# Performance work log

Measured on AMD Instinct MI355X. Metric: run time of the kernel, lower is better.

Reference implementation:

```python
import jax, jax.numpy as jnp
import numpy as np

B = 8192          # sessions
DOCS = 10         # docs per session
NPS = 21          # nodes per session: 1 query + 10 docs + 10 titles
N = B * NPS       # 172032 total nodes
F_IN, F_HID, F_OUT = 171, 256, 128


def _gat_conv(x, src, dst, W, a_src, a_dst, bias, n_nodes):
    # PyG GATConv, heads=1, negative_slope=0.2, self-loops already appended.
    h = x @ W.T                                   # [N, F]
    e = jax.nn.leaky_relu(jnp.take(h @ a_src, src) + jnp.take(h @ a_dst, dst), 0.2)
    m = jax.ops.segment_max(e, dst, num_segments=n_nodes)
    ex = jnp.exp(e - m[dst])
    denom = jax.ops.segment_sum(ex, dst, num_segments=n_nodes)
    alpha = ex / denom[dst]                       # softmax over incoming edges
    out = jax.ops.segment_sum(h[src] * alpha[:, None], dst, num_segments=n_nodes)
    return out + bias


def setup_inputs() -> dict:
    key = jax.random.key(0)
    ks = jax.random.split(key, 20)
    # structured node ids: per session block [q, d0..d9, t0..t9]
    base = jnp.arange(B, dtype=jnp.int64) * NPS
    doc_id = base[:, None] + 1 + jnp.arange(DOCS, dtype=jnp.int64)   # [B,10]
    q = base                                                          # query node = doc_id[:,0]-1
    t = doc_id + DOCS                                                 # title node = doc+10
    qd_s = jnp.repeat(q, DOCS); qd_d = doc_id.reshape(-1)
    dt_s = doc_id.reshape(-1);  dt_d = t.reshape(-1)
    src = jnp.concatenate([qd_s, qd_d, dt_s, dt_d])
    dst = jnp.concatenate([qd_d, qd_s, dt_d, dt_s])
    edge_index = jnp.stack([src, dst])                                # [2, 327680]

    inp = {
        "i": 0,
        "x": jax.random.normal(ks[0], (N, F_IN), jnp.float32),
        "edge_index": edge_index,
        "doc_id": doc_id,
        "click": jax.random.randint(ks[1], (B,), 0, 2),
        "query": jax.random.randint(ks[2], (B,), 0, 6338),
        "docu": jax.random.randint(ks[3], (B, DOCS), 0, 56477),
        "title_id": jax.random.randint(ks[4], (B, DOCS), 0, 56363),
        # embedding tables
        "query_table": jax.random.normal(ks[5], (6338, 160), jnp.float32) * 0.02,
        "doc_table": jax.random.normal(ks[6], (56477, 160), jnp.float32) * 0.02,
        "title_table": jax.random.normal(ks[7], (56363, 160), jnp.float32) * 0.02,
        "pos_table": jax.random.normal(ks[8], (10, 1), jnp.float32) * 0.02,
        "click_table": jax.random.normal(ks[9], (2, 1), jnp.float32) * 0.02,
        # GATConv 1 (171 -> 256)
        "W1": jax.random.normal(ks[10], (F_HID, F_IN), jnp.float32) * (1.0 / np.sqrt(F_IN)),
        "a_src1": jax.random.normal(ks[11], (F_HID,), jnp.float32) * 0.1,
        "a_dst1": jax.random.normal(ks[12], (F_HID,), jnp.float32) * 0.1,
        "b1": jnp.zeros((F_HID,), jnp.float32),
        # GATConv 2 (256 -> 128)
        "W2": jax.random.normal(ks[13], (F_OUT, F_HID), jnp.float32) * (1.0 / np.sqrt(F_HID)),
        "a_src2": jax.random.normal(ks[14], (F_OUT,), jnp.float32) * 0.1,
        "a_dst2": jax.random.normal(ks[15], (F_OUT,), jnp.float32) * 0.1,
        "b2": jnp.zeros((F_OUT,), jnp.float32),
        # head linear (128 -> 1)
        "Wl": jax.random.normal(ks[16], (1, F_OUT), jnp.float32) * (1.0 / np.sqrt(F_OUT)),
        "bl": jnp.zeros((1,), jnp.float32),
    }
    return inp


def reference(i, x, edge_index, doc_id, click, query, docu, title_id,
              query_table, doc_table, title_table, pos_table, click_table,
              W1, a_src1, a_dst1, b1, W2, a_src2, a_dst2, b2, Wl, bl):
    n_nodes = x.shape[0]
    q_emb = query_table[query]          # [B,160]
    d_emb = doc_table[docu]             # [B,10,160]
    t_emb = title_table[title_id]       # [B,10,160]
    pos = pos_table[:, 0]               # [10]  (position_embedding of 0..9)
    clk = click_table[click, 0]         # [B]

    df = doc_id.reshape(-1)             # flat doc node ids [B*10]
    if i == 0:
        x = x.at[doc_id[:, 0] - 1, :160].set(q_emb)
        x = x.at[df, :160].set(d_emb.reshape(-1, 160))
        x = x.at[df, 160].set(jnp.broadcast_to(pos, doc_id.shape).reshape(-1))
        x = x.at[df, 161 + i].set(jnp.broadcast_to(clk[:, None], doc_id.shape).reshape(-1))
        x = x.at[df + 10, :160].set(t_emb.reshape(-1, 160))
    else:
        x = x.at[df, 161 + i].set(jnp.broadcast_to(clk[:, None], doc_id.shape).reshape(-1))

    # add self-loops (PyG GATConv default)
    loop = jnp.arange(n_nodes, dtype=edge_index.dtype)
    src = jnp.concatenate([edge_index[0], loop])
    dst = jnp.concatenate([edge_index[1], loop])

    y = _gat_conv(x, src, dst, W1, a_src1, a_dst1, b1, n_nodes)
    y = jax.nn.relu(y)                  # dropout is identity in eval mode
    hidden_state = _gat_conv(y, src, dst, W2, a_src2, a_dst2, b2, n_nodes)
    y = jax.nn.relu(hidden_state)
    y = jax.nn.sigmoid(y @ Wl.T + bl)   # [N,1]
    return (hidden_state, y, x[:, :171])
```

## Files before the change

### kernel.cpp

```cpp
#include <hip/hip_runtime.h>
#include <cstdint>

#define N_NODES 172032
#define BATCH   8192
#define NPS     21
#define F_IN    171
#define K1P     192
#define F_HID   256
#define F_OUT   128
#define SX_F    (NPS * F_IN)
#define SXB     (NPS * K1P)
#define SPB     3
#define NBLK    2731

typedef unsigned short u16;
typedef __attribute__((ext_vector_type(8))) short  bf16x8;
typedef __attribute__((ext_vector_type(4))) float  f32x4;

__device__ inline u16 f2bf(float f) {
    unsigned u = __float_as_uint(f);
    unsigned r = u + 0x7FFFu + ((u >> 16) & 1u);
    return (u16)(r >> 16);
}
__device__ inline float bf2f(u16 h) { return __uint_as_float(((unsigned)h) << 16); }
__device__ inline float lrelu(float v) { return v > 0.f ? v : 0.2f * v; }

__device__ inline int deg_of(int n)  { return n == 0 ? 11 : (n <= 10 ? 3 : 2); }
__device__ inline int edge_base(int n) { return n == 0 ? 0 : (n <= 10 ? 11 + 3*(n-1) : 41 + 2*(n-11)); }
__device__ inline int src_of(int n, int k) {
    if (n == 0)  return k < 10 ? k + 1 : 0;
    if (n <= 10) return k == 0 ? 0 : (k == 1 ? n + 10 : n);
    return k == 0 ? n - 10 : n;
}

__device__ inline float wave_red(float v) {
    for (int off = 32; off; off >>= 1) v += __shfl_down(v, off);
    return v;
}

__global__ __launch_bounds__(256) void build_x(const int* __restrict__ iptr, const float* __restrict__ x,
                        const int* __restrict__ click, const int* __restrict__ query,
                        const int* __restrict__ docu, const int* __restrict__ title_id,
                        const float* __restrict__ qtab, const float* __restrict__ dtab,
                        const float* __restrict__ ttab, const float* __restrict__ ptab,
                        const float* __restrict__ ctab,
                        const float* __restrict__ W1, const float* __restrict__ W2,
                        float* __restrict__ out_x, u16* __restrict__ xb,
                        u16* __restrict__ W1b, u16* __restrict__ W2b)
{
    if (blockIdx.x >= BATCH) {
        int id = (blockIdx.x - BATCH) * 256 + threadIdx.x;
        if (id < 256 * K1P) {
            int r = id / K1P, k = id - r * K1P;
            W1b[id] = (k < F_IN) ? f2bf(W1[r * F_IN + k]) : (u16)0;
        }
        if (id < 128 * 256) W2b[id] = f2bf(W2[id]);
        return;
    }

    __shared__ float sx[SX_F];
    __shared__ int   dz[10], tz[10], s_q;
    __shared__ float s_clk;

    const int s   = blockIdx.x;
    const int tid = threadIdx.x;
    const int i   = iptr[0];
    const long xbase = (long)s * SX_F;

    if (tid < 10)       dz[tid]      = docu[s*10 + tid];
    else if (tid < 20)  tz[tid - 10] = title_id[s*10 + tid - 10];
    else if (tid == 20) s_q          = query[s];
    else if (tid == 21) s_clk        = ctab[click[s]];
    __syncthreads();

    if (i == 0) {
        for (int idx = tid; idx < SX_F; idx += 256) {
            int p = idx / F_IN;
            int c = idx - p * F_IN;
            float v;
            if (c >= 160) {
                if (p >= 1 && p <= 10 && c == 160)      v = ptab[p - 1];
                else if (p >= 1 && p <= 10 && c == 161) v = s_clk;
                else                                     v = x[xbase + idx];
            } else {
                if (p == 0)       v = qtab[(long)s_q * 160 + c];
                else if (p <= 10) v = dtab[(long)dz[p-1] * 160 + c];
                else              v = ttab[(long)tz[p-11] * 160 + c];
            }
            sx[idx] = v;
        }
    } else {
        for (int idx = tid; idx < SX_F; idx += 256) {
            int p = idx / F_IN;
            int c = idx - p * F_IN;
            float v = x[xbase + idx];
            if (p >= 1 && p <= 10 && c == 161 + i) v = s_clk;
            sx[idx] = v;
        }
    }
    __syncthreads();

    {
        int r    = (int)(xbase & 3);
        int head = (4 - r) & 3;
        if (tid < head) out_x[xbase + tid] = sx[tid];
        int n4 = (SX_F - head) >> 2;
        for (int id = tid; id < n4; id += 256) {
            int o = head + id * 4;
            float4 v = make_float4(sx[o], sx[o+1], sx[o+2], sx[o+3]);
            *(float4*)(out_x + xbase + o) = v;
        }
        int done = head + n4 * 4;
        int tail = SX_F - done;
        if (tid < tail) out_x[xbase + done + tid] = sx[done + tid];
    }

    {
        u16* xbs = xb + (long)s * SXB;
        for (int id = tid; id < SXB / 8; id += 256) {
            int k0 = id * 8;
            int node = k0 / K1P;
            int kk   = k0 - node * K1P;
            union { u16 h[8]; uint4 v; } u;
            #pragma unroll
            for (int j = 0; j < 8; ++j) {
                int c = kk + j;
                u.h[j] = (c < F_IN) ? f2bf(sx[node * F_IN + c]) : (u16)0;
            }
            *(uint4*)(xbs + k0) = u.v;
        }
    }
}

__global__ __launch_bounds__(256) void fused1(const u16* __restrict__ xb, const u16* __restrict__ W1b,
                                              const float* __restrict__ asrc, const float* __restrict__ adst,
                                              const float* __restrict__ bias, u16* __restrict__ y1b)
{
    constexpr int KS  = 64;
    constexpr int SA  = 200;
    constexpr int SB  = 72;
    __shared__ __align__(16) u16 Al[64 * SA];
    __shared__ __align__(16) u16 Bu[256 * SB];
    __shared__ float s_l[64], d_l[64], alpha[3 * 61];

    const int blk = blockIdx.x, tid = threadIdx.x;
    const int s0  = blk * SPB;
    const int nsamp = (s0 + SPB <= BATCH) ? SPB : (BATCH - s0);
    const int nrow  = nsamp * NPS;

    const int lane = tid & 63, w = tid >> 6;
    const int wr = w >> 1, wc = w & 1;
    const int lm = lane & 15, lq = lane >> 4;

    const u16* Ag = xb + (long)s0 * SXB;
    for (int id = tid; id < 64 * (K1P / 8); id += 256) {
        int row = id / 24, ch = id - row * 24;
        uint4 v;
        if (row < nrow) v = *(const uint4*)(Ag + row * K1P + ch * 8);
        else            v = make_uint4(0u, 0u, 0u, 0u);
        *(uint4*)(Al + row * SA + ch * 8) = v;
    }

    f32x4 acc[2][8];
    #pragma unroll
    for (int f = 0; f < 2; ++f)
        #pragma unroll
        for (int g = 0; g < 8; ++g)
            acc[f][g] = (f32x4){0.f, 0.f, 0.f, 0.f};

    for (int ks = 0; ks < K1P; ks += KS) {
        __syncthreads();
        for (int id = tid; id < 256 * (KS / 8); id += 256) {
            int row = id >> 3, ch = id & 7;
            *(uint4*)(Bu + row * SB + ch * 8) = *(const uint4*)(W1b + row * K1P + ks + ch * 8);
        }
        __syncthreads();
        #pragma unroll
        for (int kb = 0; kb < KS / 32; ++kb) {
            int ka    = ks + kb * 32 + lq * 8;
            int kboff = kb * 32 + lq * 8;
            bf16x8 a0 = *(const bf16x8*)(Al + (wr*32 +  0 + lm) * SA + ka);
            bf16x8 a1 = *(const bf16x8*)(Al + (wr*32 + 16 + lm) * SA + ka);
            #pragma unroll
            for (int g = 0; g < 8; ++g) {
                bf16x8 b = *(const bf16x8*)(Bu + (wc*128 + g*16 + lm) * SB + kboff);
                acc[0][g] = __builtin_amdgcn_mfma_f32_16x16x32_bf16(a0, b, acc[0][g], 0, 0, 0);
                acc[1][g] = __builtin_amdgcn_mfma_f32_16x16x32_bf16(a1, b, acc[1][g], 0, 0, 0);
            }
        }
    }

    __syncthreads();
    u16* h = Bu;
    #pragma unroll
    for (int f = 0; f < 2; ++f)
        #pragma unroll
        for (int g = 0; g < 8; ++g)
            #pragma unroll
            for (int r = 0; r < 4; ++r) {
                int row = wr*32 + f*16 + lq*4 + r;
                int col = wc*128 + g*16 + lm;
                h[row * F_HID + col] = f2bf(acc[f][g][r]);
            }
    __syncthreads();

    float av[4], dv[4];
    #pragma unroll
    for (int j = 0; j < 4; ++j) { av[j] = asrc[lane + j*64]; dv[j] = adst[lane + j*64]; }
    for (int n = w; n < nrow; n += 4) {
        float as_ = 0.f, ad_ = 0.f;
        #pragma unroll
        for (int j = 0; j < 4; ++j) {
            float hv = bf2f(h[n * F_HID + lane + j*64]);
            as_ += hv * av[j];
            ad_ += hv * dv[j];
        }
        as_ = wave_red(as_); ad_ = wave_red(ad_);
        if (lane == 0) { s_l[n] = as_; d_l[n] = ad_; }
    }
    __syncthreads();

    if (tid < nrow) {
        int s = tid / NPS, p = tid - s * NPS;
        int deg = deg_of(p), eb = edge_base(p);
        const float* sl = s_l + s * NPS;
        float dn = d_l[tid], m = -1e30f;
        for (int k = 0; k < deg; ++k) m = fmaxf(m, lrelu(sl[src_of(p,k)] + dn));
        float den = 0.f;
        for (int k = 0; k < deg; ++k) den += expf(lrelu(sl[src_of(p,k)] + dn) - m);
        float inv = 1.f / den;
        for (int k = 0; k < deg; ++k) alpha[s*61 + eb + k] = expf(lrelu(sl[src_of(p,k)] + dn) - m) * inv;
    }
    __syncthreads();

    const int c = tid;
    float bc = bias[c];
    for (int s = 0; s < nsamp; ++s) {
        const u16* hs = h + s * NPS * F_HID;
        const float* al = alpha + s * 61;
        u16* outp = y1b + ((long)(s0 + s) * NPS) * F_HID;
        {
            float a = al[10] * bf2f(hs[c]);
            #pragma unroll
            for (int j = 1; j <= 10; ++j) a += al[j-1] * bf2f(hs[j * F_HID + c]);
            outp[c] = f2bf(fmaxf(a + bc, 0.f));
        }
        #pragma unroll
        for (int j = 1; j <= 10; ++j) {
            int eb = 11 + 3*(j-1);
            float a = al[eb]   * bf2f(hs[c])
                    + al[eb+1] * bf2f(hs[(j+10) * F_HID + c])
                    + al[eb+2] * bf2f(hs[j * F_HID + c]);
            outp[j * F_HID + c] = f2bf(fmaxf(a + bc, 0.f));
        }
        #pragma unroll
        for (int j = 1; j <= 10; ++j) {
            int eb = 41 + 2*(j-1);
            float a = al[eb]   * bf2f(hs[j * F_HID + c])
                    + al[eb+1] * bf2f(hs[(10+j) * F_HID + c]);
            outp[(10+j) * F_HID + c] = f2bf(fmaxf(a + bc, 0.f));
        }
    }
}

__global__ __launch_bounds__(256) void fused2(const u16* __restrict__ y1b, const u16* __restrict__ W2b,
                                              const float* __restrict__ asrc, const float* __restrict__ adst,
                                              const float* __restrict__ bias,
                                              const float* __restrict__ Wl, const float* __restrict__ bl,
                                              float* __restrict__ out_hid, float* __restrict__ out_y)
{
    constexpr int KS  = 64;
    constexpr int SA  = 264;
    constexpr int SB  = 72;
    __shared__ __align__(16) u16 Al[64 * SA];
    __shared__ __align__(16) u16 Bu[128 * SB];
    __shared__ float s_l[64], d_l[64], alpha[3 * 61];

    const int blk = blockIdx.x, tid = threadIdx.x;
    const int s0  = blk * SPB;
    const int nsamp = (s0 + SPB <= BATCH) ? SPB : (BATCH - s0);
    const int nrow  = nsamp * NPS;

    const int lane = tid & 63, w = tid >> 6;
    const int wr = w >> 1, wc = w & 1;
    const int lm = lane & 15, lq = lane >> 4;

    const u16* Ag = y1b + (long)s0 * NPS * F_HID;
    for (int id = tid; id < 64 * (F_HID / 8); id += 256) {
        int row = id >> 5, ch = id & 31;
        uint4 v;
        if (row < nrow) v = *(const uint4*)(Ag + row * F_HID + ch * 8);
        else            v = make_uint4(0u, 0u, 0u, 0u);
        *(uint4*)(Al + row * SA + ch * 8) = v;
    }

    f32x4 acc[2][4];
    #pragma unroll
    for (int f = 0; f < 2; ++f)
        #pragma unroll
        for (int g = 0; g < 4; ++g)
            acc[f][g] = (f32x4){0.f, 0.f, 0.f, 0.f};

    for (int ks = 0; ks < F_HID; ks += KS) {
        __syncthreads();
        for (int id = tid; id < 128 * (KS / 8); id += 256) {
            int row = id >> 3, ch = id & 7;
            *(uint4*)(Bu + row * SB + ch * 8) = *(const uint4*)(W2b + row * F_HID + ks + ch * 8);
        }
        __syncthreads();
        #pragma unroll
        for (int kb = 0; kb < KS / 32; ++kb) {
            int ka    = ks + kb * 32 + lq * 8;
            int kboff = kb * 32 + lq * 8;
            bf16x8 a0 = *(const bf16x8*)(Al + (wr*32 +  0 + lm) * SA + ka);
            bf16x8 a1 = *(const bf16x8*)(Al + (wr*32 + 16 + lm) * SA + ka);
            #pragma unroll
            for (int g = 0; g < 4; ++g) {
                bf16x8 b = *(const bf16x8*)(Bu + (wc*64 + g*16 + lm) * SB + kboff);
                acc[0][g] = __builtin_amdgcn_mfma_f32_16x16x32_bf16(a0, b, acc[0][g], 0, 0, 0);
                acc[1][g] = __builtin_amdgcn_mfma_f32_16x16x32_bf16(a1, b, acc[1][g], 0, 0, 0);
            }
        }
    }

    __syncthreads();
    u16* h2 = Bu;
    #pragma unroll
    for (int f = 0; f < 2; ++f)
        #pragma unroll
        for (int g = 0; g < 4; ++g)
            #pragma unroll
            for (int r = 0; r < 4; ++r) {
                int row = wr*32 + f*16 + lq*4 + r;
                int col = wc*64 + g*16 + lm;
                h2[row * F_OUT + col] = f2bf(acc[f][g][r]);
            }
    __syncthreads();

    float av[2], dv[2];
    #pragma unroll
    for (int j = 0; j < 2; ++j) { av[j] = asrc[lane + j*64]; dv[j] = adst[lane + j*64]; }
    for (int n = w; n < nrow; n += 4) {
        float as_ = 0.f, ad_ = 0.f;
        #pragma unroll
        for (int j = 0; j < 2; ++j) {
            float hv = bf2f(h2[n * F_OUT + lane + j*64]);
            as_ += hv * av[j];
            ad_ += hv * dv[j];
        }
        as_ = wave_red(as_); ad_ = wave_red(ad_);
        if (lane == 0) { s_l[n] = as_; d_l[n] = ad_; }
    }
    __syncthreads();

    if (tid < nrow) {
        int s = tid / NPS, p = tid - s * NPS;
        int deg = deg_of(p), eb = edge_base(p);
        const float* sl = s_l + s * NPS;
        float dn = d_l[tid], m = -1e30f;
        for (int k = 0; k < deg; ++k) m = fmaxf(m, lrelu(sl[src_of(p,k)] + dn));
        float den = 0.f;
        for (int k = 0; k < deg; ++k) den += expf(lrelu(sl[src_of(p,k)] + dn) - m);
        float inv = 1.f / den;
        for (int k = 0; k < deg; ++k) alpha[s*61 + eb + k] = expf(lrelu(sl[src_of(p,k)] + dn) - m) * inv;
    }
    __syncthreads();

    float* hidwl = (float*)Al;
    const int c    = tid & 127;
    const int half = tid >> 7;
    float bc = bias[c];
    float wl = Wl[c];
    for (int s = 0; s < nsamp; ++s) {
        const u16* hs = h2 + s * NPS * F_OUT;
        const float* al = alpha + s * 61;
        long gb = (long)(s0 + s) * NPS * F_OUT;
        for (int p = half; p < NPS; p += 2) {
            int deg = deg_of(p), eb = edge_base(p);
            float a = 0.f;
            for (int k = 0; k < deg; ++k) a += al[eb + k] * bf2f(hs[src_of(p,k) * F_OUT + c]);
            float hv = a + bc;
            out_hid[gb + p * F_OUT + c] = hv;
            hidwl[(s * NPS + p) * F_OUT + c] = fmaxf(hv, 0.f) * wl;
        }
    }
    __syncthreads();

    float bl0 = bl[0];
    for (int n = w; n < nrow; n += 4) {
        float v = hidwl[n * F_OUT + lane] + hidwl[n * F_OUT + lane + 64];
        v = wave_red(v);
        if (lane == 0) out_y[(long)s0 * NPS + n] = 1.f / (1.f + expf(-(v + bl0)));
    }
}

extern "C" void kernel_launch(void* const* d_in, const int* in_sizes, int n_in,
                              void* d_out, int out_size, void* d_ws, size_t ws_size,
                              hipStream_t stream) {
    const int*   ip    = (const int*)  d_in[0];
    const float* x     = (const float*)d_in[1];
    const int*   click = (const int*)  d_in[4];
    const int*   query = (const int*)  d_in[5];
    const int*   docu  = (const int*)  d_in[6];
    const int*   title = (const int*)  d_in[7];
    const float* qtab  = (const float*)d_in[8];
    const float* dtab  = (const float*)d_in[9];
    const float* ttab  = (const float*)d_in[10];
    const float* ptab  = (const float*)d_in[11];
    const float* ctab  = (const float*)d_in[12];
    const float* W1    = (const float*)d_in[13];
    const float* as1   = (const float*)d_in[14];
    const float* ad1   = (const float*)d_in[15];
    const float* b1    = (const float*)d_in[16];
    const float* W2    = (const float*)d_in[17];
    const float* as2   = (const float*)d_in[18];
    const float* ad2   = (const float*)d_in[19];
    const float* b2    = (const float*)d_in[20];
    const float* Wl    = (const float*)d_in[21];
    const float* bl    = (const float*)d_in[22];

    float* out_hid = (float*)d_out;
    float* out_y   = out_hid + (long)N_NODES * F_OUT;
    float* out_x   = out_y + N_NODES;

    u16* xb  = (u16*)d_ws;
    u16* y1b = xb + (long)BATCH * SXB;
    u16* W1b = y1b + (long)N_NODES * F_HID;
    u16* W2b = W1b + 256 * K1P;

    build_x<<<BATCH + 192, 256, 0, stream>>>(ip, x, click, query, docu, title,
                                             qtab, dtab, ttab, ptab, ctab,
                                             W1, W2, out_x, xb, W1b, W2b);
    fused1<<<NBLK, 256, 0, stream>>>(xb, W1b, as1, ad1, b1, y1b);
    fused2<<<NBLK, 256, 0, stream>>>(y1b, W2b, as2, ad2, b2, Wl, bl, out_hid, out_y);
}
```

Measured before the change: 645.5 us.

## Read GEMM weights from global memory, fuse attention logits into epilogue, pad LDS

Both fused GAT kernels stop staging weight tiles through shared memory with a sync-heavy k loop. They now read W1b/W2b fragments directly from global memory or L2, and shared memory holds only the activation tile, so occupancy can rise (launch bounds now request 4 blocks). The attention source and destination dot products are computed from MFMA accumulators with shuffle reductions instead of a separate pass over LDS, and the softmax caches exponentials. The prep kernel pads the shared row stride and gathers embeddings with float4 loads, and the final linear head reduces per wave without an extra LDS buffer. In exchange, each wave repeatedly fetches weights from global memory, which relies on cache hits.

```diff
diff --git a/kernel.cpp b/kernel.cpp
--- a/kernel.cpp
+++ b/kernel.cpp
@@ -9,6 +9,7 @@
 #define F_HID   256
 #define F_OUT   128
 #define SX_F    (NPS * F_IN)
+#define SXP     172
 #define SXB     (NPS * K1P)
 #define SPB     3
 #define NBLK    2731
@@ -58,7 +59,7 @@
         return;
     }
 
-    __shared__ float sx[SX_F];
+    __shared__ float sx[NPS * SXP];
     __shared__ int   dz[10], tz[10], s_q;
     __shared__ float s_clk;
 
@@ -74,20 +75,21 @@
     __syncthreads();
 
     if (i == 0) {
-        for (int idx = tid; idx < SX_F; idx += 256) {
-            int p = idx / F_IN;
-            int c = idx - p * F_IN;
+        for (int id = tid; id < NPS * 40; id += 256) {
+            int p = id / 40, c4 = (id - p * 40) * 4;
+            const float* src;
+            if (p == 0)       src = qtab + (long)s_q * 160;
+            else if (p <= 10) src = dtab + (long)dz[p-1] * 160;
+            else              src = ttab + (long)tz[p-11] * 160;
+            *(float4*)(sx + p * SXP + c4) = *(const float4*)(src + c4);
+        }
+        for (int id = tid; id < NPS * 11; id += 256) {
+            int p = id / 11, c = 160 + (id - p * 11);
             float v;
-            if (c >= 160) {
-                if (p >= 1 && p <= 10 && c == 160)      v = ptab[p - 1];
-                else if (p >= 1 && p <= 10 && c == 161) v = s_clk;
-                else                                     v = x[xbase + idx];
-            } else {
-                if (p == 0)       v = qtab[(long)s_q * 160 + c];
-                else if (p <= 10) v = dtab[(long)dz[p-1] * 160 + c];
-                else              v = ttab[(long)tz[p-11] * 160 + c];
-            }
-            sx[idx] = v;
+            if (p >= 1 && p <= 10 && c == 160)      v = ptab[p - 1];
+            else if (p >= 1 && p <= 10 && c == 161) v = s_clk;
+            else                                     v = x[xbase + p * F_IN + c];
+            sx[p * SXP + c] = v;
         }
     } else {
         for (int idx = tid; idx < SX_F; idx += 256) {
@@ -95,7 +97,7 @@
             int c = idx - p * F_IN;
             float v = x[xbase + idx];
             if (p >= 1 && p <= 10 && c == 161 + i) v = s_clk;
-            sx[idx] = v;
+            sx[p * SXP + c] = v;
         }
     }
     __syncthreads();
@@ -103,16 +105,33 @@
     {
         int r    = (int)(xbase & 3);
         int head = (4 - r) & 3;
-        if (tid < head) out_x[xbase + tid] = sx[tid];
+        if (tid < head) {
+            int p = tid / F_IN, c = tid - p * F_IN;
+            out_x[xbase + tid] = sx[p * SXP + c];
+        }
         int n4 = (SX_F - head) >> 2;
         for (int id = tid; id < n4; id += 256) {
             int o = head + id * 4;
-            float4 v = make_float4(sx[o], sx[o+1], sx[o+2], sx[o+3]);
+            float4 v;
+            {
+                int p0 = o / F_IN, c0 = o - p0 * F_IN;
+                v.x = sx[p0 * SXP + c0];
+                int o1 = o + 1; int p1 = o1 / F_IN, c1 = o1 - p1 * F_IN;
+                v.y = sx[p1 * SXP + c1];
+                int o2 = o + 2; int p2 = o2 / F_IN, c2 = o2 - p2 * F_IN;
+                v.z = sx[p2 * SXP + c2];
+                int o3 = o + 3; int p3 = o3 / F_IN, c3 = o3 - p3 * F_IN;
+                v.w = sx[p3 * SXP + c3];
+            }
             *(float4*)(out_x + xbase + o) = v;
         }
         int done = head + n4 * 4;
         int tail = SX_F - done;
-        if (tid < tail) out_x[xbase + done + tid] = sx[done + tid];
+        if (tid < tail) {
+            int idx = done + tid;
+            int p = idx / F_IN, c = idx - p * F_IN;
+            out_x[xbase + idx] = sx[p * SXP + c];
+        }
     }
 
     {
@@ -125,23 +144,21 @@
             #pragma unroll
             for (int j = 0; j < 8; ++j) {
                 int c = kk + j;
-                u.h[j] = (c < F_IN) ? f2bf(sx[node * F_IN + c]) : (u16)0;
+                u.h[j] = (c < F_IN) ? f2bf(sx[node * SXP + c]) : (u16)0;
             }
             *(uint4*)(xbs + k0) = u.v;
         }
     }
 }
 
-__global__ __launch_bounds__(256) void fused1(const u16* __restrict__ xb, const u16* __restrict__ W1b,
-                                              const float* __restrict__ asrc, const float* __restrict__ adst,
-                                              const float* __restrict__ bias, u16* __restrict__ y1b)
+__global__ __launch_bounds__(256, 4) void fused1(const u16* __restrict__ xb, const u16* __restrict__ W1b,
+                                                 const float* __restrict__ asrc, const float* __restrict__ adst,
+                                                 const float* __restrict__ bias, u16* __restrict__ y1b)
 {
-    constexpr int KS  = 64;
-    constexpr int SA  = 200;
-    constexpr int SB  = 72;
-    __shared__ __align__(16) u16 Al[64 * SA];
-    __shared__ __align__(16) u16 Bu[256 * SB];
-    __shared__ float s_l[64], d_l[64], alpha[3 * 61];
+    constexpr int SA = 200;
+    __shared__ __align__(16) u16 hbuf[64 * 256];
+    __shared__ float s_part[2][64], d_part[2][64];
+    __shared__ float alpha[SPB * 61];
 
     const int blk = blockIdx.x, tid = threadIdx.x;
     const int s0  = blk * SPB;
@@ -153,13 +170,14 @@
     const int lm = lane & 15, lq = lane >> 4;
 
     const u16* Ag = xb + (long)s0 * SXB;
-    for (int id = tid; id < 64 * (K1P / 8); id += 256) {
+    for (int id = tid; id < 64 * 24; id += 256) {
         int row = id / 24, ch = id - row * 24;
         uint4 v;
         if (row < nrow) v = *(const uint4*)(Ag + row * K1P + ch * 8);
         else            v = make_uint4(0u, 0u, 0u, 0u);
-        *(uint4*)(Al + row * SA + ch * 8) = v;
-    }
+        *(uint4*)(hbuf + row * SA + ch * 8) = v;
+    }
+    __syncthreads();
 
     f32x4 acc[2][8];
     #pragma unroll
@@ -168,68 +186,65 @@
         for (int g = 0; g < 8; ++g)
             acc[f][g] = (f32x4){0.f, 0.f, 0.f, 0.f};
 
-    for (int ks = 0; ks < K1P; ks += KS) {
-        __syncthreads();
-        for (int id = tid; id < 256 * (KS / 8); id += 256) {
-            int row = id >> 3, ch = id & 7;
-            *(uint4*)(Bu + row * SB + ch * 8) = *(const uint4*)(W1b + row * K1P + ks + ch * 8);
-        }
-        __syncthreads();
-        #pragma unroll
-        for (int kb = 0; kb < KS / 32; ++kb) {
-            int ka    = ks + kb * 32 + lq * 8;
-            int kboff = kb * 32 + lq * 8;
-            bf16x8 a0 = *(const bf16x8*)(Al + (wr*32 +  0 + lm) * SA + ka);
-            bf16x8 a1 = *(const bf16x8*)(Al + (wr*32 + 16 + lm) * SA + ka);
+    #pragma unroll
+    for (int kb = 0; kb < K1P / 32; ++kb) {
+        int koff = kb * 32 + lq * 8;
+        bf16x8 a0 = *(const bf16x8*)(hbuf + (wr*32 +  0 + lm) * SA + koff);
+        bf16x8 a1 = *(const bf16x8*)(hbuf + (wr*32 + 16 + lm) * SA + koff);
+        #pragma unroll
+        for (int g = 0; g < 8; ++g) {
+            bf16x8 b = *(const bf16x8*)(W1b + (wc*128 + g*16 + lm) * K1P + koff);
+            acc[0][g] = __builtin_amdgcn_mfma_f32_16x16x32_bf16(a0, b, acc[0][g], 0, 0, 0);
+            acc[1][g] = __builtin_amdgcn_mfma_f32_16x16x32_bf16(a1, b, acc[1][g], 0, 0, 0);
+        }
+    }
+    __syncthreads();
+
+    u16* h = hbuf;
+    float av[8], dv[8];
+    #pragma unroll
+    for (int g = 0; g < 8; ++g) {
+        av[g] = asrc[wc*128 + g*16 + lm];
+        dv[g] = adst[wc*128 + g*16 + lm];
+    }
+    #pragma unroll
+    for (int f = 0; f < 2; ++f)
+        #pragma unroll
+        for (int r = 0; r < 4; ++r) {
+            int row = wr*32 + f*16 + lq*4 + r;
+            float sp = 0.f, dp = 0.f;
             #pragma unroll
             for (int g = 0; g < 8; ++g) {
-                bf16x8 b = *(const bf16x8*)(Bu + (wc*128 + g*16 + lm) * SB + kboff);
-                acc[0][g] = __builtin_amdgcn_mfma_f32_16x16x32_bf16(a0, b, acc[0][g], 0, 0, 0);
-                acc[1][g] = __builtin_amdgcn_mfma_f32_16x16x32_bf16(a1, b, acc[1][g], 0, 0, 0);
-            }
-        }
-    }
-
-    __syncthreads();
-    u16* h = Bu;
-    #pragma unroll
-    for (int f = 0; f < 2; ++f)
-        #pragma unroll
-        for (int g = 0; g < 8; ++g)
-            #pragma unroll
-            for (int r = 0; r < 4; ++r) {
-                int row = wr*32 + f*16 + lq*4 + r;
-                int col = wc*128 + g*16 + lm;
-                h[row * F_HID + col] = f2bf(acc[f][g][r]);
-            }
-    __syncthreads();
-
-    float av[4], dv[4];
-    #pragma unroll
-    for (int j = 0; j < 4; ++j) { av[j] = asrc[lane + j*64]; dv[j] = adst[lane + j*64]; }
-    for (int n = w; n < nrow; n += 4) {
-        float as_ = 0.f, ad_ = 0.f;
-        #pragma unroll
-        for (int j = 0; j < 4; ++j) {
-            float hv = bf2f(h[n * F_HID + lane + j*64]);
-            as_ += hv * av[j];
-            ad_ += hv * dv[j];
-        }
-        as_ = wave_red(as_); ad_ = wave_red(ad_);
-        if (lane == 0) { s_l[n] = as_; d_l[n] = ad_; }
-    }
+                float v = acc[f][g][r];
+                h[row * F_HID + wc*128 + g*16 + lm] = f2bf(v);
+                sp += v * av[g];
+                dp += v * dv[g];
+            }
+            #pragma unroll
+            for (int off = 1; off < 16; off <<= 1) {
+                sp += __shfl_xor(sp, off);
+                dp += __shfl_xor(dp, off);
+            }
+            if (lm == 0) { s_part[wc][row] = sp; d_part[wc][row] = dp; }
+        }
     __syncthreads();
 
     if (tid < nrow) {
         int s = tid / NPS, p = tid - s * NPS;
         int deg = deg_of(p), eb = edge_base(p);
-        const float* sl = s_l + s * NPS;
-        float dn = d_l[tid], m = -1e30f;
-        for (int k = 0; k < deg; ++k) m = fmaxf(m, lrelu(sl[src_of(p,k)] + dn));
+        int sb = s * NPS;
+        float dn = d_part[0][tid] + d_part[1][tid];
+        float e[11];
+        float m = -1e30f;
+        for (int k = 0; k < deg; ++k) {
+            int sn = sb + src_of(p, k);
+            e[k] = lrelu(s_part[0][sn] + s_part[1][sn] + dn);
+            m = fmaxf(m, e[k]);
+        }
         float den = 0.f;
-        for (int k = 0; k < deg; ++k) den += expf(lrelu(sl[src_of(p,k)] + dn) - m);
+        for (int k = 0; k < deg; ++k) { e[k] = expf(e[k] - m); den += e[k]; }
         float inv = 1.f / den;
-        for (int k = 0; k < deg; ++k) alpha[s*61 + eb + k] = expf(lrelu(sl[src_of(p,k)] + dn) - m) * inv;
+        for (int k = 0; k < deg; ++k) alpha[s*61 + eb + k] = e[k] * inv;
     }
     __syncthreads();
 
@@ -263,18 +278,17 @@
     }
 }
 
-__global__ __launch_bounds__(256) void fused2(const u16* __restrict__ y1b, const u16* __restrict__ W2b,
-                                              const float* __restrict__ asrc, const float* __restrict__ adst,
-                                              const float* __restrict__ bias,
-                                              const float* __restrict__ Wl, const float* __restrict__ bl,
-                                              float* __restrict__ out_hid, float* __restrict__ out_y)
+__global__ __launch_bounds__(256, 4) void fused2(const u16* __restrict__ y1b, const u16* __restrict__ W2b,
+                                                 const float* __restrict__ asrc, const float* __restrict__ adst,
+                                                 const float* __restrict__ bias,
+                                                 const float* __restrict__ Wl, const float* __restrict__ bl,
+                                                 float* __restrict__ out_hid, float* __restrict__ out_y)
 {
-    constexpr int KS  = 64;
-    constexpr int SA  = 264;
-    constexpr int SB  = 72;
-    __shared__ __align__(16) u16 Al[64 * SA];
-    __shared__ __align__(16) u16 Bu[128 * SB];
-    __shared__ float s_l[64], d_l[64], alpha[3 * 61];
+    constexpr int SA = 264;
+    __shared__ __align__(16) u16 hbuf[64 * SA];
+    __shared__ float s_part[2][64], d_part[2][64];
+    __shared__ float alpha[SPB * 61];
+    __shared__ float rpart[SPB * NPS][2];
 
     const int blk = blockIdx.x, tid = threadIdx.x;
     const int s0  = blk * SPB;
@@ -286,13 +300,14 @@
     const int lm = lane & 15, lq = lane >> 4;
 
     const u16* Ag = y1b + (long)s0 * NPS * F_HID;
-    for (int id = tid; id < 64 * (F_HID / 8); id += 256) {
+    for (int id = tid; id < 64 * 32; id += 256) {
         int row = id >> 5, ch = id & 31;
         uint4 v;
         if (row < nrow) v = *(const uint4*)(Ag + row * F_HID + ch * 8);
         else            v = make_uint4(0u, 0u, 0u, 0u);
-        *(uint4*)(Al + row * SA + ch * 8) = v;
-    }
+        *(uint4*)(hbuf + row * SA + ch * 8) = v;
+    }
+    __syncthreads();
 
     f32x4 acc[2][4];
     #pragma unroll
@@ -301,72 +316,68 @@
         for (int g = 0; g < 4; ++g)
             acc[f][g] = (f32x4){0.f, 0.f, 0.f, 0.f};
 
-    for (int ks = 0; ks < F_HID; ks += KS) {
-        __syncthreads();
-        for (int id = tid; id < 128 * (KS / 8); id += 256) {
-            int row = id >> 3, ch = id & 7;
-            *(uint4*)(Bu + row * SB + ch * 8) = *(const uint4*)(W2b + row * F_HID + ks + ch * 8);
-        }
-        __syncthreads();
-        #pragma unroll
-        for (int kb = 0; kb < KS / 32; ++kb) {
-            int ka    = ks + kb * 32 + lq * 8;
-            int kboff = kb * 32 + lq * 8;
-            bf16x8 a0 = *(const bf16x8*)(Al + (wr*32 +  0 + lm) * SA + ka);
-            bf16x8 a1 = *(const bf16x8*)(Al + (wr*32 + 16 + lm) * SA + ka);
+    #pragma unroll
+    for (int kb = 0; kb < F_HID / 32; ++kb) {
+        int koff = kb * 32 + lq * 8;
+        bf16x8 a0 = *(const bf16x8*)(hbuf + (wr*32 +  0 + lm) * SA + koff);
+        bf16x8 a1 = *(const bf16x8*)(hbuf + (wr*32 + 16 + lm) * SA + koff);
+        #pragma unroll
+        for (int g = 0; g < 4; ++g) {
+            bf16x8 b = *(const bf16x8*)(W2b + (wc*64 + g*16 + lm) * F_HID + koff);
+            acc[0][g] = __builtin_amdgcn_mfma_f32_16x16x32_bf16(a0, b, acc[0][g], 0, 0, 0);
+            acc[1][g] = __builtin_amdgcn_mfma_f32_16x16x32_bf16(a1, b, acc[1][g], 0, 0, 0);
+        }
+    }
+    __syncthreads();
+
+    u16* h2 = hbuf;
+    float av[4], dv[4];
+    #pragma unroll
+    for (int g = 0; g < 4; ++g) {
+        av[g] = asrc[wc*64 + g*16 + lm];
+        dv[g] = adst[wc*64 + g*16 + lm];
+    }
+    #pragma unroll
+    for (int f = 0; f < 2; ++f)
+        #pragma unroll
+        for (int r = 0; r < 4; ++r) {
+            int row = wr*32 + f*16 + lq*4 + r;
+            float sp = 0.f, dp = 0.f;
             #pragma unroll
             for (int g = 0; g < 4; ++g) {
-                bf16x8 b = *(const bf16x8*)(Bu + (wc*64 + g*16 + lm) * SB + kboff);
-                acc[0][g] = __builtin_amdgcn_mfma_f32_16x16x32_bf16(a0, b, acc[0][g], 0, 0, 0);
-                acc[1][g] = __builtin_amdgcn_mfma_f32_16x16x32_bf16(a1, b, acc[1][g], 0, 0, 0);
-            }
-        }
-    }
-
-    __syncthreads();
-    u16* h2 = Bu;
-    #pragma unroll
-    for (int f = 0; f < 2; ++f)
-        #pragma unroll
-        for (int g = 0; g < 4; ++g)
-            #pragma unroll
-            for (int r = 0; r < 4; ++r) {
-                int row = wr*32 + f*16 + lq*4 + r;
-                int col = wc*64 + g*16 + lm;
-                h2[row * F_OUT + col] = f2bf(acc[f][g][r]);
-            }
-    __syncthreads();
-
-    float av[2], dv[2];
-    #pragma unroll
-    for (int j = 0; j < 2; ++j) { av[j] = asrc[lane + j*64]; dv[j] = adst[lane + j*64]; }
-    for (int n = w; n < nrow; n += 4) {
-        float as_ = 0.f, ad_ = 0.f;
-        #pragma unroll
-        for (int j = 0; j < 2; ++j) {
-            float hv = bf2f(h2[n * F_OUT + lane + j*64]);
-            as_ += hv * av[j];
-            ad_ += hv * dv[j];
-        }
-        as_ = wave_red(as_); ad_ = wave_red(ad_);
-        if (lane == 0) { s_l[n] = as_; d_l[n] = ad_; }
-    }
+                float v = acc[f][g][r];
+                h2[row * F_OUT + wc*64 + g*16 + lm] = f2bf(v);
+                sp += v * av[g];
+                dp += v * dv[g];
+            }
+            #pragma unroll
+            for (int off = 1; off < 16; off <<= 1) {
+                sp += __shfl_xor(sp, off);
+                dp += __shfl_xor(dp, off);
+            }
+            if (lm == 0) { s_part[wc][row] = sp; d_part[wc][row] = dp; }
+        }
     __syncthreads();
 
     if (tid < nrow) {
         int s = tid / NPS, p = tid - s * NPS;
         int deg = deg_of(p), eb = edge_base(p);
-        const float* sl = s_l + s * NPS;
-        float dn = d_l[tid], m = -1e30f;
-        for (int k = 0; k < deg; ++k) m = fmaxf(m, lrelu(sl[src_of(p,k)] + dn));
+        int sb = s * NPS;
+        float dn = d_part[0][tid] + d_part[1][tid];
+        float e[11];
+        float m = -1e30f;
+        for (int k = 0; k < deg; ++k) {
+            int sn = sb + src_of(p, k);
+            e[k] = lrelu(s_part[0][sn] + s_part[1][sn] + dn);
+            m = fmaxf(m, e[k]);
+        }
         float den = 0.f;
-        for (int k = 0; k < deg; ++k) den += expf(lrelu(sl[src_of(p,k)] + dn) - m);
+        for (int k = 0; k < deg; ++k) { e[k] = expf(e[k] - m); den += e[k]; }
         float inv = 1.f / den;
-        for (int k = 0; k < deg; ++k) alpha[s*61 + eb + k] = expf(lrelu(sl[src_of(p,k)] + dn) - m) * inv;
-    }
-    __syncthreads();
-
-    float* hidwl = (float*)Al;
+        for (int k = 0; k < deg; ++k) alpha[s*61 + eb + k] = e[k] * inv;
+    }
+    __syncthreads();
+
     const int c    = tid & 127;
     const int half = tid >> 7;
     float bc = bias[c];
@@ -381,16 +392,15 @@
             for (int k = 0; k < deg; ++k) a += al[eb + k] * bf2f(hs[src_of(p,k) * F_OUT + c]);
             float hv = a + bc;
             out_hid[gb + p * F_OUT + c] = hv;
-            hidwl[(s * NPS + p) * F_OUT + c] = fmaxf(hv, 0.f) * wl;
-        }
-    }
-    __syncthreads();
-
-    float bl0 = bl[0];
-    for (int n = w; n < nrow; n += 4) {
-        float v = hidwl[n * F_OUT + lane] + hidwl[n * F_OUT + lane + 64];
-        v = wave_red(v);
-        if (lane == 0) out_y[(long)s0 * NPS + n] = 1.f / (1.f + expf(-(v + bl0)));
+            float rv = wave_red(fmaxf(hv, 0.f) * wl);
+            if (lane == 0) rpart[s * NPS + p][w & 1] = rv;
+        }
+    }
+    __syncthreads();
+
+    if (tid < nrow) {
+        float v = rpart[tid][0] + rpart[tid][1] + bl[0];
+        out_y[(long)s0 * NPS + tid] = 1.f / (1.f + expf(-v));
     }
 }
 
```

After: 571.1 us. -11.5%, faster.
